# Performance work log

Hardware: AMD Instinct MI355X
Metric: run time of the kernel (lower is better)

Reference implementation:

```python
import jax, jax.numpy as jnp
import numpy as np

N = 100000   # nodes
E = 1600000  # edges (avg degree 16)
DIN = 128
DH = 64


def setup_inputs() -> dict:
    key = jax.random.key(0)
    ks = jax.random.split(key, 6)
    x = jax.random.normal(ks[0], (N, DIN), dtype=jnp.float32)
    edge_index = jax.random.randint(ks[1], (2, E), 0, N, dtype=jnp.int32)
    W1 = jax.random.normal(ks[2], (DIN, DH), dtype=jnp.float32) * (1.0 / np.sqrt(DIN))
    b1 = jnp.zeros((DH,), dtype=jnp.float32)
    W2 = jax.random.normal(ks[3], (DH, DH), dtype=jnp.float32) * (1.0 / np.sqrt(DH))
    b2 = jnp.zeros((DH,), dtype=jnp.float32)
    alpha = jnp.full((DH,), 0.25, dtype=jnp.float32)  # PReLU per-channel slope (torch default 0.25)
    return {"x": x, "edge_index": edge_index, "W1": W1, "b1": b1, "W2": W2, "b2": b2, "alpha": alpha}


def _gcn_layer(h, src, dst, norm, W, b):
    # GCNConv: linear transform, then normalized scatter-add aggregation, then bias
    h = h @ W                                  # [N, dout]
    msg = h[src] * norm[:, None]               # [E+N, dout] gathered + scaled messages
    agg = jax.ops.segment_sum(msg, dst, num_segments=N)
    return agg + b


def reference(x, edge_index, W1, b1, W2, b2, alpha):
    src0, dst0 = edge_index[0], edge_index[1]
    # GCNConv default: add self-loops, symmetric normalization deg^{-1/2} A deg^{-1/2}
    loops = jnp.arange(N, dtype=src0.dtype)
    src = jnp.concatenate([src0, loops])
    dst = jnp.concatenate([dst0, loops])
    ones = jnp.ones(src.shape[0], dtype=x.dtype)
    deg = jax.ops.segment_sum(ones, dst, num_segments=N)
    dinv = jnp.where(deg > 0, jax.lax.rsqrt(deg), 0.0)
    norm = dinv[src] * dinv[dst]               # [E+N]

    prelu = lambda z: jnp.where(z >= 0, z, alpha * z)  # shared per-channel PReLU
    z = prelu(_gcn_layer(x, src, dst, norm, W1, b1))
    z = prelu(_gcn_layer(z, src, dst, norm, W2, b2))
    return z
```

## Files before the change

### kernel.cpp

```cpp
#include <hip/hip_runtime.h>
#include <hip/hip_bf16.h>

#define NN 100000
#define NE 1600000
#define NBUCK 391
#define CAP 5120
#define CHUNK 2048
#define PBLOCKS 782
#define MMBLOCKS 1563

typedef __attribute__((ext_vector_type(8))) short short8;
typedef __attribute__((ext_vector_type(4))) float f32x4;

static __device__ __forceinline__ unsigned short f2bf(float f) {
    unsigned u = __float_as_uint(f);
    unsigned r = (u + 0x7fffu + ((u >> 16) & 1u)) >> 16;
    return (unsigned short)r;
}
static __device__ __forceinline__ float bf_lo(unsigned u) {
    return __uint_as_float(u << 16);
}
static __device__ __forceinline__ float bf_hi(unsigned u) {
    return __uint_as_float(u & 0xffff0000u);
}
static __device__ __forceinline__ void acc8(float* acc, uint4 v, float nm) {
    acc[0] += bf_lo(v.x) * nm; acc[1] += bf_hi(v.x) * nm;
    acc[2] += bf_lo(v.y) * nm; acc[3] += bf_hi(v.y) * nm;
    acc[4] += bf_lo(v.z) * nm; acc[5] += bf_hi(v.z) * nm;
    acc[6] += bf_lo(v.w) * nm; acc[7] += bf_hi(v.w) * nm;
}

static __device__ __forceinline__ void agg_loop(const unsigned short* hc,
                                                const int* __restrict__ esrc,
                                                const float* __restrict__ dinv,
                                                int start, int cnt, float dn,
                                                float* acc) {
    int i = 0;
    for (; i + 4 <= cnt; i += 4) {
        int s0 = esrc[start + i];
        int s1 = esrc[start + i + 1];
        int s2 = esrc[start + i + 2];
        int s3 = esrc[start + i + 3];
        float n0 = dinv[s0] * dn, n1 = dinv[s1] * dn;
        float n2 = dinv[s2] * dn, n3 = dinv[s3] * dn;
        uint4 w0 = *(const uint4*)(hc + (long)s0 * 64);
        uint4 w1 = *(const uint4*)(hc + (long)s1 * 64);
        uint4 w2 = *(const uint4*)(hc + (long)s2 * 64);
        uint4 w3 = *(const uint4*)(hc + (long)s3 * 64);
        acc8(acc, w0, n0); acc8(acc, w1, n1); acc8(acc, w2, n2); acc8(acc, w3, n3);
    }
    for (; i < cnt; ++i) {
        int s0 = esrc[start + i];
        float n0 = dinv[s0] * dn;
        uint4 w0 = *(const uint4*)(hc + (long)s0 * 64);
        acc8(acc, w0, n0);
    }
}

__global__ __launch_bounds__(256) void k_fat(const int* __restrict__ ei,
                                             int* __restrict__ bcur,
                                             unsigned* __restrict__ ebuf,
                                             const float* __restrict__ x,
                                             const float* __restrict__ W1,
                                             unsigned short* __restrict__ hout) {
    __shared__ __attribute__((aligned(16))) unsigned char smem[17408];
    int tid = threadIdx.x;
    if (blockIdx.x < PBLOCKS) {
        int* lh = (int*)smem;
        int* lbase = lh + NBUCK;
        int e0 = blockIdx.x * CHUNK;
        for (int i = tid; i < NBUCK; i += 256) lh[i] = 0;
        __syncthreads();
        int bs[8]; int rs[8]; unsigned ps[8];
        #pragma unroll
        for (int k = 0; k < 8; ++k) {
            int e = e0 + k * 256 + tid;
            bs[k] = -1;
            if (e < NE) {
                int d = ei[NE + e];
                int s = ei[e];
                int b = d >> 8;
                bs[k] = b;
                rs[k] = atomicAdd(&lh[b], 1);
                ps[k] = ((unsigned)s << 8) | (unsigned)(d & 255);
            }
        }
        __syncthreads();
        for (int i = tid; i < NBUCK; i += 256) {
            int c = lh[i];
            lbase[i] = c ? atomicAdd(&bcur[i], c) : 0;
        }
        __syncthreads();
        #pragma unroll
        for (int k = 0; k < 8; ++k) {
            if (bs[k] >= 0) {
                int pos = lbase[bs[k]] + rs[k];
                if (pos < CAP)
                    ebuf[(long)bs[k] * CAP + pos] = ps[k];
            }
        }
    } else {
        constexpr int K = 128, KP = K + 8;
        unsigned short* Wt = (unsigned short*)smem;
        for (int idx = tid; idx < K * 64; idx += 256) {
            int k = idx >> 6, n = idx & 63;
            Wt[n * KP + k] = f2bf(W1[idx]);
        }
        __syncthreads();
        int wave = tid >> 6, lane = tid & 63;
        int m = lane & 15, q = lane >> 4;
        int n0 = (blockIdx.x - PBLOCKS) * 64 + wave * 16;
        f32x4 acc[4] = {{0.f,0.f,0.f,0.f},{0.f,0.f,0.f,0.f},{0.f,0.f,0.f,0.f},{0.f,0.f,0.f,0.f}};
        int row = n0 + m;
        int rowc = row < NN ? row : NN - 1;
        const float* xr = x + (long)rowc * K;
        #pragma unroll
        for (int kk = 0; kk < K / 32; ++kk) {
            const float4* p = (const float4*)(xr + kk * 32 + q * 8);
            float4 v0 = p[0], v1 = p[1];
            float xv[8] = {v0.x, v0.y, v0.z, v0.w, v1.x, v1.y, v1.z, v1.w};
            short8 afrag;
            #pragma unroll
            for (int i2 = 0; i2 < 8; ++i2) afrag[i2] = (short)f2bf(xv[i2]);
            #pragma unroll
            for (int nt = 0; nt < 4; ++nt) {
                const short8* bp = (const short8*)&Wt[(nt * 16 + m) * KP + kk * 32 + q * 8];
                acc[nt] = __builtin_amdgcn_mfma_f32_16x16x32_bf16(afrag, *bp, acc[nt], 0, 0, 0);
            }
        }
        #pragma unroll
        for (int reg = 0; reg < 4; ++reg) {
            int node = n0 + q * 4 + reg;
            if (node < NN) {
                #pragma unroll
                for (int nt = 0; nt < 4; ++nt)
                    hout[(long)node * 64 + nt * 16 + m] = f2bf(acc[nt][reg]);
            }
        }
    }
}

__global__ __launch_bounds__(256) void k_build(const int* __restrict__ bcur,
                                               const unsigned* __restrict__ ebuf,
                                               unsigned* __restrict__ rowinfo,
                                               float* __restrict__ dinv,
                                               int* __restrict__ esrc) {
    __shared__ int cnt[2048];
    __shared__ int kstart[2048];
    __shared__ int wsum[4];
    int tid = threadIdx.x;
    int base = blockIdx.x * CAP;
    int nedge = bcur[blockIdx.x];
    if (nedge > CAP) nedge = CAP;
    #pragma unroll
    for (int t = 0; t < 8; ++t) cnt[(tid << 3) | t] = 0;
    __syncthreads();
    int st[20];
    int ssrc[20];
    #pragma unroll
    for (int k = 0; k < 20; ++k) {
        int j = tid + k * 256;
        st[k] = -1;
        if (j < nedge) {
            unsigned p = ebuf[base + j];
            int dl = (int)(p & 255u);
            int s = (int)(p >> 8);
            int key = (dl << 3) | (s >> 14);
            int r = atomicAdd(&cnt[key], 1);
            st[k] = (r << 11) | key;
            ssrc[k] = s;
        }
    }
    __syncthreads();
    int c[8];
    int v = 0;
    #pragma unroll
    for (int t = 0; t < 8; ++t) { c[t] = cnt[(tid << 3) | t]; v += c[t]; }
    int lane = tid & 63;
    int incl = v;
    #pragma unroll
    for (int off = 1; off < 64; off <<= 1) {
        int t = __shfl_up(incl, off, 64);
        if (lane >= off) incl += t;
    }
    if (lane == 63) wsum[tid >> 6] = incl;
    __syncthreads();
    if (tid == 0) {
        int a = 0;
        #pragma unroll
        for (int w = 0; w < 4; ++w) { int t = wsum[w]; wsum[w] = a; a += t; }
    }
    __syncthreads();
    int ex = incl - v + wsum[tid >> 6];
    int node = blockIdx.x * 256 + tid;
    if (node < NN) {
        rowinfo[node] = ((unsigned)(base + ex) << 11) | (unsigned)v;
        dinv[node] = rsqrtf((float)(v + 1));
    }
    int off = base + ex;
    #pragma unroll
    for (int t = 0; t < 8; ++t) { kstart[(tid << 3) | t] = off; off += c[t]; }
    __syncthreads();
    #pragma unroll
    for (int k = 0; k < 20; ++k) {
        if (st[k] >= 0)
            esrc[kstart[st[k] & 2047] + (st[k] >> 11)] = ssrc[k];
    }
}

__global__ __launch_bounds__(256) void k_aggmm(const unsigned* __restrict__ rowinfo,
                                               const int* __restrict__ esrc,
                                               const unsigned short* __restrict__ h,
                                               const float* __restrict__ dinv,
                                               const float* __restrict__ bias,
                                               const float* __restrict__ alpha,
                                               const float* __restrict__ W2,
                                               unsigned short* __restrict__ hout2) {
    __shared__ unsigned short Wt[64 * 72];
    __shared__ unsigned short aggs[32 * 72];
    int tid = threadIdx.x;
    for (int idx = tid; idx < 64 * 64; idx += 256) {
        int k = idx >> 6, n = idx & 63;
        Wt[n * 72 + k] = f2bf(W2[idx]);
    }
    int sl = tid & 7;
    int ln = tid >> 3;
    int node = blockIdx.x * 32 + ln;
    unsigned u = rowinfo[node];
    int start = (int)(u >> 11);
    int cnt = (int)(u & 2047u);
    float dn = dinv[node];
    const unsigned short* hc = h + sl * 8;

    float acc[8];
    {
        uint4 hw = *(const uint4*)(hc + (long)node * 64);
        float d2 = dn * dn;
        acc[0] = bf_lo(hw.x) * d2; acc[1] = bf_hi(hw.x) * d2;
        acc[2] = bf_lo(hw.y) * d2; acc[3] = bf_hi(hw.y) * d2;
        acc[4] = bf_lo(hw.z) * d2; acc[5] = bf_hi(hw.z) * d2;
        acc[6] = bf_lo(hw.w) * d2; acc[7] = bf_hi(hw.w) * d2;
    }
    agg_loop(hc, esrc, dinv, start, cnt, dn, acc);

    float4 blo = *(const float4*)(bias + sl * 8);
    float4 bhi = *(const float4*)(bias + sl * 8 + 4);
    float4 alo = *(const float4*)(alpha + sl * 8);
    float4 ahi = *(const float4*)(alpha + sl * 8 + 4);
    float bb[8] = {blo.x, blo.y, blo.z, blo.w, bhi.x, bhi.y, bhi.z, bhi.w};
    float aa[8] = {alo.x, alo.y, alo.z, alo.w, ahi.x, ahi.y, ahi.z, ahi.w};
    #pragma unroll
    for (int j = 0; j < 8; ++j) {
        float v = acc[j] + bb[j];
        acc[j] = v >= 0.f ? v : aa[j] * v;
    }
    uint4 pk;
    pk.x = (unsigned)f2bf(acc[0]) | ((unsigned)f2bf(acc[1]) << 16);
    pk.y = (unsigned)f2bf(acc[2]) | ((unsigned)f2bf(acc[3]) << 16);
    pk.z = (unsigned)f2bf(acc[4]) | ((unsigned)f2bf(acc[5]) << 16);
    pk.w = (unsigned)f2bf(acc[6]) | ((unsigned)f2bf(acc[7]) << 16);
    *(uint4*)&aggs[ln * 72 + sl * 8] = pk;
    __syncthreads();

    int wave = tid >> 6;
    if (wave < 2) {
        int lane = tid & 63;
        int m = lane & 15, q = lane >> 4;
        int row = wave * 16 + m;
        f32x4 c2[4] = {{0.f,0.f,0.f,0.f},{0.f,0.f,0.f,0.f},{0.f,0.f,0.f,0.f},{0.f,0.f,0.f,0.f}};
        #pragma unroll
        for (int kk = 0; kk < 2; ++kk) {
            short8 afrag = *(const short8*)&aggs[row * 72 + kk * 32 + q * 8];
            #pragma unroll
            for (int nt = 0; nt < 4; ++nt) {
                const short8* bp = (const short8*)&Wt[(nt * 16 + m) * 72 + kk * 32 + q * 8];
                c2[nt] = __builtin_amdgcn_mfma_f32_16x16x32_bf16(afrag, *bp, c2[nt], 0, 0, 0);
            }
        }
        #pragma unroll
        for (int reg = 0; reg < 4; ++reg) {
            int nd = blockIdx.x * 32 + wave * 16 + q * 4 + reg;
            #pragma unroll
            for (int nt = 0; nt < 4; ++nt)
                hout2[(long)nd * 64 + nt * 16 + m] = f2bf(c2[nt][reg]);
        }
    }
}

__global__ __launch_bounds__(256) void k_agg2(const unsigned* __restrict__ rowinfo,
                                              const int* __restrict__ esrc,
                                              const unsigned short* __restrict__ h,
                                              const float* __restrict__ dinv,
                                              const float* __restrict__ bias,
                                              const float* __restrict__ alpha,
                                              float* __restrict__ out) {
    int sl = threadIdx.x & 7;
    int node = blockIdx.x * 32 + (threadIdx.x >> 3);
    unsigned u = rowinfo[node];
    int start = (int)(u >> 11);
    int cnt = (int)(u & 2047u);
    float dn = dinv[node];
    const unsigned short* hc = h + sl * 8;

    float acc[8];
    {
        uint4 hw = *(const uint4*)(hc + (long)node * 64);
        float d2 = dn * dn;
        acc[0] = bf_lo(hw.x) * d2; acc[1] = bf_hi(hw.x) * d2;
        acc[2] = bf_lo(hw.y) * d2; acc[3] = bf_hi(hw.y) * d2;
        acc[4] = bf_lo(hw.z) * d2; acc[5] = bf_hi(hw.z) * d2;
        acc[6] = bf_lo(hw.w) * d2; acc[7] = bf_hi(hw.w) * d2;
    }
    agg_loop(hc, esrc, dinv, start, cnt, dn, acc);

    float4 blo = *(const float4*)(bias + sl * 8);
    float4 bhi = *(const float4*)(bias + sl * 8 + 4);
    float4 alo = *(const float4*)(alpha + sl * 8);
    float4 ahi = *(const float4*)(alpha + sl * 8 + 4);
    float bb[8] = {blo.x, blo.y, blo.z, blo.w, bhi.x, bhi.y, bhi.z, bhi.w};
    float aa[8] = {alo.x, alo.y, alo.z, alo.w, ahi.x, ahi.y, ahi.z, ahi.w};
    #pragma unroll
    for (int j = 0; j < 8; ++j) {
        float v = acc[j] + bb[j];
        acc[j] = v >= 0.f ? v : aa[j] * v;
    }
    float* op = out + (long)node * 64 + sl * 8;
    *(float4*)op = make_float4(acc[0], acc[1], acc[2], acc[3]);
    *(float4*)(op + 4) = make_float4(acc[4], acc[5], acc[6], acc[7]);
}

extern "C" void kernel_launch(void* const* d_in, const int* in_sizes, int n_in,
                              void* d_out, int out_size, void* d_ws, size_t ws_size,
                              hipStream_t stream) {
    const float* x     = (const float*)d_in[0];
    const int*   ei    = (const int*)d_in[1];
    const float* W1    = (const float*)d_in[2];
    const float* b1    = (const float*)d_in[3];
    const float* W2    = (const float*)d_in[4];
    const float* b2    = (const float*)d_in[5];
    const float* alpha = (const float*)d_in[6];
    float* out = (float*)d_out;

    char* ws = (char*)d_ws;
    float*    dinv      = (float*)(ws);
    unsigned* rowinfo   = (unsigned*)(ws + 400384);
    int*      bcur      = (int*)(ws + 800768);
    int*      esrc      = (int*)(ws + 802816);
    unsigned short* hbf = (unsigned short*)(ws + 8810496);
    unsigned* ebuf      = (unsigned*)(ws + 21610496);
    unsigned short* hbf2 = (unsigned short*)(ws + 21610496);

    (void)hipMemsetAsync(bcur, 0, NBUCK * sizeof(int), stream);
    k_fat<<<PBLOCKS + MMBLOCKS, 256, 0, stream>>>(ei, bcur, ebuf, x, W1, hbf);
    k_build<<<NBUCK, 256, 0, stream>>>(bcur, ebuf, rowinfo, dinv, esrc);
    k_aggmm<<<NN / 32, 256, 0, stream>>>(rowinfo, esrc, hbf, dinv, b1, alpha, W2, hbf2);
    k_agg2<<<NN / 32, 256, 0, stream>>>(rowinfo, esrc, hbf2, dinv, b2, alpha, out);
}
```

Before: 227.3 us.

## Stage bucketed edges in LDS for coalesced scatter and pad bucket counters

The partition blocks now compute an in-block exclusive scan of bucket counts and write each packed edge into a shared-memory staging buffer sorted by bucket, along with its global destination. A second pass then writes the staged edges to the global bucket buffer in slot order, so consecutive threads write to contiguous runs inside each bucket instead of scattering. Each global bucket counter is padded to its own 64-byte line to cut atomic contention from false sharing. Bucket capacity shrinks slightly so the workspace layout still fits. The cost is more shared memory per block, extra barriers and the scan work.

```diff
diff --git a/kernel.cpp b/kernel.cpp
--- a/kernel.cpp
+++ b/kernel.cpp
@@ -4,10 +4,11 @@
 #define NN 100000
 #define NE 1600000
 #define NBUCK 391
-#define CAP 5120
+#define CAP 5056
 #define CHUNK 2048
 #define PBLOCKS 782
 #define MMBLOCKS 1563
+#define BCUR_STRIDE 16
 
 typedef __attribute__((ext_vector_type(8))) short short8;
 typedef __attribute__((ext_vector_type(4))) float f32x4;
@@ -63,13 +64,18 @@
                                              const float* __restrict__ x,
                                              const float* __restrict__ W1,
                                              unsigned short* __restrict__ hout) {
-    __shared__ __attribute__((aligned(16))) unsigned char smem[17408];
+    __shared__ __attribute__((aligned(16))) unsigned char smem[19584];
     int tid = threadIdx.x;
     if (blockIdx.x < PBLOCKS) {
-        int* lh = (int*)smem;
-        int* lbase = lh + NBUCK;
+        int* lexc  = (int*)smem;
+        int* lbase = (int*)(smem + 1564);
+        unsigned* sv = (unsigned*)(smem + 3128);
+        int* sd    = (int*)(smem + 11320);
+        int* wscan = (int*)(smem + 19512);
+        int* sTot  = (int*)(smem + 19528);
+
         int e0 = blockIdx.x * CHUNK;
-        for (int i = tid; i < NBUCK; i += 256) lh[i] = 0;
+        for (int i = tid; i < NBUCK; i += 256) lexc[i] = 0;
         __syncthreads();
         int bs[8]; int rs[8]; unsigned ps[8];
         #pragma unroll
@@ -81,23 +87,53 @@
                 int s = ei[e];
                 int b = d >> 8;
                 bs[k] = b;
-                rs[k] = atomicAdd(&lh[b], 1);
+                rs[k] = atomicAdd(&lexc[b], 1);
                 ps[k] = ((unsigned)s << 8) | (unsigned)(d & 255);
             }
         }
         __syncthreads();
-        for (int i = tid; i < NBUCK; i += 256) {
-            int c = lh[i];
-            lbase[i] = c ? atomicAdd(&bcur[i], c) : 0;
-        }
+        int b0i = 2 * tid, b1i = 2 * tid + 1;
+        int c0 = (b0i < NBUCK) ? lexc[b0i] : 0;
+        int c1 = (b1i < NBUCK) ? lexc[b1i] : 0;
+        int v = c0 + c1;
+        int lane = tid & 63;
+        int incl = v;
+        #pragma unroll
+        for (int off = 1; off < 64; off <<= 1) {
+            int t = __shfl_up(incl, off, 64);
+            if (lane >= off) incl += t;
+        }
+        if (lane == 63) wscan[tid >> 6] = incl;
+        int gb0 = 0, gb1 = 0;
+        if (c0) gb0 = atomicAdd(&bcur[b0i * BCUR_STRIDE], c0);
+        if (c1) gb1 = atomicAdd(&bcur[b1i * BCUR_STRIDE], c1);
+        __syncthreads();
+        if (tid == 0) {
+            int a = 0;
+            #pragma unroll
+            for (int w = 0; w < 4; ++w) { int t = wscan[w]; wscan[w] = a; a += t; }
+            *sTot = a;
+        }
+        __syncthreads();
+        int ex = incl - v + wscan[tid >> 6];
+        if (b0i < NBUCK) { lexc[b0i] = ex;      lbase[b0i] = gb0; }
+        if (b1i < NBUCK) { lexc[b1i] = ex + c0; lbase[b1i] = gb1; }
         __syncthreads();
         #pragma unroll
         for (int k = 0; k < 8; ++k) {
             if (bs[k] >= 0) {
-                int pos = lbase[bs[k]] + rs[k];
-                if (pos < CAP)
-                    ebuf[(long)bs[k] * CAP + pos] = ps[k];
-            }
+                int b = bs[k];
+                int slot = lexc[b] + rs[k];
+                int pos  = lbase[b] + rs[k];
+                sv[slot] = ps[k];
+                sd[slot] = (pos < CAP) ? b * CAP + pos : -1;
+            }
+        }
+        __syncthreads();
+        int V = *sTot;
+        for (int j = tid; j < V; j += 256) {
+            int d = sd[j];
+            if (d >= 0) ebuf[d] = sv[j];
         }
     } else {
         constexpr int K = 128, KP = K + 8;
@@ -150,7 +186,7 @@
     __shared__ int wsum[4];
     int tid = threadIdx.x;
     int base = blockIdx.x * CAP;
-    int nedge = bcur[blockIdx.x];
+    int nedge = bcur[blockIdx.x * BCUR_STRIDE];
     if (nedge > CAP) nedge = CAP;
     #pragma unroll
     for (int t = 0; t < 8; ++t) cnt[(tid << 3) | t] = 0;
@@ -345,12 +381,12 @@
     float*    dinv      = (float*)(ws);
     unsigned* rowinfo   = (unsigned*)(ws + 400384);
     int*      bcur      = (int*)(ws + 800768);
-    int*      esrc      = (int*)(ws + 802816);
-    unsigned short* hbf = (unsigned short*)(ws + 8810496);
-    unsigned* ebuf      = (unsigned*)(ws + 21610496);
-    unsigned short* hbf2 = (unsigned short*)(ws + 21610496);
-
-    (void)hipMemsetAsync(bcur, 0, NBUCK * sizeof(int), stream);
+    int*      esrc      = (int*)(ws + 825856);
+    unsigned short* hbf = (unsigned short*)(ws + 8733440);
+    unsigned* ebuf      = (unsigned*)(ws + 21533440);
+    unsigned short* hbf2 = (unsigned short*)(ws + 21533440);
+
+    (void)hipMemsetAsync(bcur, 0, NBUCK * BCUR_STRIDE * sizeof(int), stream);
     k_fat<<<PBLOCKS + MMBLOCKS, 256, 0, stream>>>(ei, bcur, ebuf, x, W1, hbf);
     k_build<<<NBUCK, 256, 0, stream>>>(bcur, ebuf, rowinfo, dinv, esrc);
     k_aggmm<<<NN / 32, 256, 0, stream>>>(rowinfo, esrc, hbf, dinv, b1, alpha, W2, hbf2);
```

After: 218.1 us. -4.1%, faster.
